# Performance work log

Hardware: AMD Instinct MI355X
Metric: run time of the kernel (lower is better)

## Reference

```python
import jax, jax.numpy as jnp
import numpy as np

D_MODEL = 1024
NHEAD = 16
WINDOW = 128


def setup_inputs() -> dict:
    key = jax.random.key(0)
    ks = jax.random.split(key, 7)
    B, L, D = 4, 4096, D_MODEL
    s = 0.02
    return {
        "q": jax.random.normal(ks[0], (B, L, D), jnp.float32),
        "k": jax.random.normal(ks[1], (B, L, D), jnp.float32),
        "v": jax.random.normal(ks[2], (B, L, D), jnp.float32),
        "in_proj_w": jax.random.normal(ks[3], (3 * D, D), jnp.float32) * s,
        "in_proj_b": jnp.zeros((3 * D,), jnp.float32),
        "out_w": jax.random.normal(ks[4], (D, D), jnp.float32) * s,
        "out_b": jnp.zeros((D,), jnp.float32),
    }


def reference(q, k, v, in_proj_w, in_proj_b, out_w, out_b):
    B, L, D = q.shape
    H, W = NHEAD, WINDOW
    hd = D // H
    nW = L // W
    Wq, Wk, Wv = in_proj_w[:D], in_proj_w[D:2 * D], in_proj_w[2 * D:]
    bq, bk, bv = in_proj_b[:D], in_proj_b[D:2 * D], in_proj_b[2 * D:]
    # shared per-window projections (same weights every window, as in nn.MultiheadAttention)
    qp = (q @ Wq.T + bq).reshape(B, nW, W, H, hd)
    kp = (k @ Wk.T + bk).reshape(B, nW, W, H, hd)
    vp = (v @ Wv.T + bv).reshape(B, nW, W, H, hd)
    scale = 1.0 / np.sqrt(hd).astype(np.float32)
    # block-diagonal attention: scores only within each window n
    scores = jnp.einsum("bnqhd,bnkhd->bnhqk", qp, kp) * scale  # [B,nW,H,W,W]
    attn = jax.nn.softmax(scores, axis=-1)
    out = jnp.einsum("bnhqk,bnkhd->bnqhd", attn, vp).reshape(B, L, D)
    return out @ out_w.T + out_b
```

## Files before the change

kernel.cpp:

```cpp
#include <hip/hip_runtime.h>


#define M_TOK 16384
#define DM    1024

typedef __bf16 bf16x8 __attribute__((ext_vector_type(8)));
typedef float  f32x4  __attribute__((ext_vector_type(4)));
typedef unsigned short us8 __attribute__((ext_vector_type(8)));
typedef unsigned short us4 __attribute__((ext_vector_type(4)));

__device__ __forceinline__ unsigned short f2bf(float f) {
    unsigned u = __float_as_uint(f);
    u += 0x7FFFu + ((u >> 16) & 1u);
    return (unsigned short)(u >> 16);
}

__global__ __launch_bounds__(256) void gemm_qkv(
    const float* __restrict__ qin, const float* __restrict__ kin,
    const float* __restrict__ vin, const float* __restrict__ ipw,
    const float* __restrict__ ipb, unsigned short* __restrict__ qkv)
{
    __shared__ unsigned short As[128 * 40];
    __shared__ unsigned short Ws[128 * 40];

    const int z = blockIdx.z;
    const float* A  = (z == 0) ? qin : ((z == 1) ? kin : vin);
    const float* Wp = ipw + (size_t)z * DM * DM;
    const float* bp = ipb + z * DM;
    unsigned short* Cp = qkv + (size_t)z * M_TOK * DM;

    const int mbase = blockIdx.y * 128;
    const int nbase = blockIdx.x * 128;
    const int tid  = threadIdx.x;
    const int lane = tid & 63;
    const int wv   = tid >> 6;
    const int wrow = (wv >> 1) * 64;
    const int wcol = (wv & 1) * 64;
    const int lrow = lane & 15;
    const int kof  = (lane >> 4) * 8;
    const int srow = tid >> 3;
    const int sc4  = tid & 7;

    f32x4 acc[4][4] = {};

    for (int ks = 0; ks < 32; ++ks) {
        const int k0 = ks * 32;
        __syncthreads();
        #pragma unroll
        for (int it = 0; it < 4; ++it) {
            int row = it * 32 + srow;
            float4 av = *(const float4*)(A  + (size_t)(mbase + row) * DM + k0 + sc4 * 4);
            float4 wf = *(const float4*)(Wp + (size_t)(nbase + row) * DM + k0 + sc4 * 4);
            us4 ap, wp4;
            ap[0] = f2bf(av.x); ap[1] = f2bf(av.y); ap[2] = f2bf(av.z); ap[3] = f2bf(av.w);
            wp4[0] = f2bf(wf.x); wp4[1] = f2bf(wf.y); wp4[2] = f2bf(wf.z); wp4[3] = f2bf(wf.w);
            *(us4*)(As + row * 40 + sc4 * 4) = ap;
            *(us4*)(Ws + row * 40 + sc4 * 4) = wp4;
        }
        __syncthreads();

        bf16x8 af[4], bfr[4];
        #pragma unroll
        for (int i = 0; i < 4; ++i)
            af[i] = *(const bf16x8*)(As + (wrow + i * 16 + lrow) * 40 + kof);
        #pragma unroll
        for (int i = 0; i < 4; ++i)
            bfr[i] = *(const bf16x8*)(Ws + (wcol + i * 16 + lrow) * 40 + kof);
        #pragma unroll
        for (int i = 0; i < 4; ++i)
            #pragma unroll
            for (int j = 0; j < 4; ++j)
                acc[i][j] = __builtin_amdgcn_mfma_f32_16x16x32_bf16(af[i], bfr[j], acc[i][j], 0, 0, 0);
    }

    #pragma unroll
    for (int j = 0; j < 4; ++j) {
        int gc = nbase + wcol + j * 16 + lrow;
        float bv = bp[gc];
        #pragma unroll
        for (int i = 0; i < 4; ++i) {
            int gr0 = mbase + wrow + i * 16 + (lane >> 4) * 4;
            #pragma unroll
            for (int r = 0; r < 4; ++r)
                Cp[(size_t)(gr0 + r) * DM + gc] = f2bf(acc[i][j][r] + bv);
        }
    }
}

__global__ __launch_bounds__(256) void gemm_out(
    const unsigned short* __restrict__ x, const float* __restrict__ ow,
    const float* __restrict__ ob, float* __restrict__ out)
{
    __shared__ unsigned short As[128 * 40];
    __shared__ unsigned short Ws[128 * 40];

    const int mbase = blockIdx.y * 128;
    const int nbase = blockIdx.x * 128;
    const int tid  = threadIdx.x;
    const int lane = tid & 63;
    const int wv   = tid >> 6;
    const int wrow = (wv >> 1) * 64;
    const int wcol = (wv & 1) * 64;
    const int lrow = lane & 15;
    const int kof  = (lane >> 4) * 8;
    const int srow = tid >> 3;
    const int sc4  = tid & 7;

    f32x4 acc[4][4] = {};

    for (int ks = 0; ks < 32; ++ks) {
        const int k0 = ks * 32;
        __syncthreads();
        #pragma unroll
        for (int it = 0; it < 4; ++it) {
            int row = it * 32 + srow;
            us4 av = *(const us4*)(x + (size_t)(mbase + row) * DM + k0 + sc4 * 4);
            float4 wf = *(const float4*)(ow + (size_t)(nbase + row) * DM + k0 + sc4 * 4);
            us4 wp4;
            wp4[0] = f2bf(wf.x); wp4[1] = f2bf(wf.y); wp4[2] = f2bf(wf.z); wp4[3] = f2bf(wf.w);
            *(us4*)(As + row * 40 + sc4 * 4) = av;
            *(us4*)(Ws + row * 40 + sc4 * 4) = wp4;
        }
        __syncthreads();

        bf16x8 af[4], bfr[4];
        #pragma unroll
        for (int i = 0; i < 4; ++i)
            af[i] = *(const bf16x8*)(As + (wrow + i * 16 + lrow) * 40 + kof);
        #pragma unroll
        for (int i = 0; i < 4; ++i)
            bfr[i] = *(const bf16x8*)(Ws + (wcol + i * 16 + lrow) * 40 + kof);
        #pragma unroll
        for (int i = 0; i < 4; ++i)
            #pragma unroll
            for (int j = 0; j < 4; ++j)
                acc[i][j] = __builtin_amdgcn_mfma_f32_16x16x32_bf16(af[i], bfr[j], acc[i][j], 0, 0, 0);
    }

    #pragma unroll
    for (int j = 0; j < 4; ++j) {
        int gc = nbase + wcol + j * 16 + lrow;
        float bv = ob[gc];
        #pragma unroll
        for (int i = 0; i < 4; ++i) {
            int gr0 = mbase + wrow + i * 16 + (lane >> 4) * 4;
            #pragma unroll
            for (int r = 0; r < 4; ++r)
                out[(size_t)(gr0 + r) * DM + gc] = acc[i][j][r] + bv;
        }
    }
}

__global__ __launch_bounds__(256) void attn_win(
    const unsigned short* __restrict__ qkv, unsigned short* __restrict__ aout)
{
    const unsigned short* qp = qkv;
    const unsigned short* kp = qkv + (size_t)M_TOK * DM;
    const unsigned short* vp = qkv + 2 * (size_t)M_TOK * DM;

    const int gid = blockIdx.x;
    const int h  = gid & 15;
    const int wi = (gid >> 4) & 31;
    const int b  = gid >> 9;
    const size_t rowbase = (size_t)b * 4096 + (size_t)wi * 128;

    const int tid  = threadIdx.x;
    const int lane = tid & 63;
    const int wv   = tid >> 6;
    const int lrow = lane & 15;
    const int kof  = (lane >> 4) * 8;

    __shared__ unsigned short sm[27136];
    unsigned short* Qs = sm;
    unsigned short* Ks = sm + 9216;
    unsigned short* Vt = sm + 18432;
    unsigned short* Ps = sm;

    {
        const int seg = tid & 7;
        #pragma unroll
        for (int it = 0; it < 4; ++it) {
            int r = it * 32 + (tid >> 3);
            size_t g = (rowbase + r) * DM + h * 64 + seg * 8;
            *(int4*)(Qs + r * 72 + seg * 8) = *(const int4*)(qp + g);
            *(int4*)(Ks + r * 72 + seg * 8) = *(const int4*)(kp + g);
        }
        #pragma unroll
        for (int it = 0; it < 4; ++it) {
            int j  = tid & 127;
            int sg = it * 2 + (tid >> 7);
            us8 vv = *(const us8*)(vp + (rowbase + j) * DM + h * 64 + sg * 8);
            #pragma unroll
            for (int d = 0; d < 8; ++d)
                Vt[(sg * 8 + d) * 136 + j] = vv[d];
        }
    }
    __syncthreads();

    f32x4 acc[2][8] = {};
    #pragma unroll
    for (int ki = 0; ki < 2; ++ki) {
        bf16x8 a0 = *(const bf16x8*)(Qs + (wv * 32 +  0 + lrow) * 72 + ki * 32 + kof);
        bf16x8 a1 = *(const bf16x8*)(Qs + (wv * 32 + 16 + lrow) * 72 + ki * 32 + kof);
        #pragma unroll
        for (int ni = 0; ni < 8; ++ni) {
            bf16x8 bb = *(const bf16x8*)(Ks + (ni * 16 + lrow) * 72 + ki * 32 + kof);
            acc[0][ni] = __builtin_amdgcn_mfma_f32_16x16x32_bf16(a0, bb, acc[0][ni], 0, 0, 0);
            acc[1][ni] = __builtin_amdgcn_mfma_f32_16x16x32_bf16(a1, bb, acc[1][ni], 0, 0, 0);
        }
    }

    const float scale = 0.125f;
    #pragma unroll
    for (int mi = 0; mi < 2; ++mi) {
        #pragma unroll
        for (int r = 0; r < 4; ++r) {
            float sc[8];
            float mx = -3.4e38f;
            #pragma unroll
            for (int ni = 0; ni < 8; ++ni) { sc[ni] = acc[mi][ni][r] * scale; mx = fmaxf(mx, sc[ni]); }
            mx = fmaxf(mx, __shfl_xor(mx, 1));
            mx = fmaxf(mx, __shfl_xor(mx, 2));
            mx = fmaxf(mx, __shfl_xor(mx, 4));
            mx = fmaxf(mx, __shfl_xor(mx, 8));
            float sum = 0.f;
            #pragma unroll
            for (int ni = 0; ni < 8; ++ni) { sc[ni] = __expf(sc[ni] - mx); sum += sc[ni]; }
            sum += __shfl_xor(sum, 1);
            sum += __shfl_xor(sum, 2);
            sum += __shfl_xor(sum, 4);
            sum += __shfl_xor(sum, 8);
            float inv = 1.0f / sum;
            #pragma unroll
            for (int ni = 0; ni < 8; ++ni) acc[mi][ni][r] = sc[ni] * inv;
        }
    }

    __syncthreads();

    #pragma unroll
    for (int mi = 0; mi < 2; ++mi)
        #pragma unroll
        for (int ni = 0; ni < 8; ++ni)
            #pragma unroll
            for (int r = 0; r < 4; ++r)
                Ps[(wv * 32 + mi * 16 + (lane >> 4) * 4 + r) * 136 + ni * 16 + lrow] =
                    f2bf(acc[mi][ni][r]);
    __syncthreads();

    f32x4 o[2][4] = {};
    #pragma unroll
    for (int kj = 0; kj < 4; ++kj) {
        bf16x8 a0 = *(const bf16x8*)(Ps + (wv * 32 +  0 + lrow) * 136 + kj * 32 + kof);
        bf16x8 a1 = *(const bf16x8*)(Ps + (wv * 32 + 16 + lrow) * 136 + kj * 32 + kof);
        #pragma unroll
        for (int nd = 0; nd < 4; ++nd) {
            bf16x8 bb = *(const bf16x8*)(Vt + (nd * 16 + lrow) * 136 + kj * 32 + kof);
            o[0][nd] = __builtin_amdgcn_mfma_f32_16x16x32_bf16(a0, bb, o[0][nd], 0, 0, 0);
            o[1][nd] = __builtin_amdgcn_mfma_f32_16x16x32_bf16(a1, bb, o[1][nd], 0, 0, 0);
        }
    }

    #pragma unroll
    for (int mi = 0; mi < 2; ++mi) {
        #pragma unroll
        for (int nd = 0; nd < 4; ++nd) {
            #pragma unroll
            for (int r = 0; r < 4; ++r) {
                int R = wv * 32 + mi * 16 + (lane >> 4) * 4 + r;
                int c = h * 64 + nd * 16 + lrow;
                aout[(rowbase + R) * DM + c] = f2bf(o[mi][nd][r]);
            }
        }
    }
}

extern "C" void kernel_launch(void* const* d_in, const int* in_sizes, int n_in,
                              void* d_out, int out_size, void* d_ws, size_t ws_size,
                              hipStream_t stream) {
    const float* q   = (const float*)d_in[0];
    const float* k   = (const float*)d_in[1];
    const float* v   = (const float*)d_in[2];
    const float* ipw = (const float*)d_in[3];
    const float* ipb = (const float*)d_in[4];
    const float* ow  = (const float*)d_in[5];
    const float* ob  = (const float*)d_in[6];
    float* out = (float*)d_out;

    unsigned short* qkv = (unsigned short*)d_ws;
    const size_t qkv_elems = 3ull * M_TOK * DM;
    const size_t need_full = (qkv_elems + (size_t)M_TOK * DM) * 2;
    unsigned short* aout = (ws_size >= need_full) ? qkv + qkv_elems : qkv;

    gemm_qkv<<<dim3(8, 128, 3), 256, 0, stream>>>(q, k, v, ipw, ipb, qkv);
    attn_win<<<dim3(2048), 256, 0, stream>>>(qkv, aout);
    gemm_out<<<dim3(8, 128), 256, 0, stream>>>(aout, ow, ob, out);
}
```

Baseline: 542.1 us.

## Pre-convert inputs to bf16, use direct global-to-LDS GEMM loads and head-major QKV layout

```diff
diff --git a/kernel.cpp b/kernel.cpp
--- a/kernel.cpp
+++ b/kernel.cpp
@@ -1,5 +1,4 @@
 #include <hip/hip_runtime.h>
-
 
 #define M_TOK 16384
 #define DM    1024
@@ -15,34 +14,241 @@
     return (unsigned short)(u >> 16);
 }
 
-__global__ __launch_bounds__(256) void gemm_qkv(
+__device__ __forceinline__ void gl2lds16(const unsigned short* g, unsigned short* l) {
+    __builtin_amdgcn_global_load_lds(
+        (const __attribute__((address_space(1))) unsigned int*)g,
+        (__attribute__((address_space(3))) unsigned int*)l, 16, 0, 0);
+}
+
+__global__ __launch_bounds__(256) void conv_f2b(
+    const float* __restrict__ src, unsigned short* __restrict__ dst, int n8)
+{
+    int i = blockIdx.x * blockDim.x + threadIdx.x;
+    int stride = gridDim.x * blockDim.x;
+    for (; i < n8; i += stride) {
+        const float4* s = (const float4*)(src + (size_t)i * 8);
+        float4 a = s[0], b = s[1];
+        us8 o;
+        o[0] = f2bf(a.x); o[1] = f2bf(a.y); o[2] = f2bf(a.z); o[3] = f2bf(a.w);
+        o[4] = f2bf(b.x); o[5] = f2bf(b.y); o[6] = f2bf(b.z); o[7] = f2bf(b.w);
+        *(us8*)(dst + (size_t)i * 8) = o;
+    }
+}
+
+#define GEMM_CORE(A_, B_)                                                      \
+    __shared__ unsigned short As[4096];                                        \
+    __shared__ unsigned short Bs[4096];                                        \
+    const int tid = threadIdx.x, lane = tid & 63, wv = tid >> 6;               \
+    const int wrow = (wv >> 1) * 64, wcol = (wv & 1) * 64;                     \
+    const int lrow = lane & 15, qd = lane >> 4;                                \
+    const int mbase = blockIdx.y * 128, nbase = blockIdx.x * 128;              \
+    const int s0 = tid, s1 = tid + 256;                                        \
+    const int r0 = s0 >> 2, c0 = (s0 & 3) ^ ((r0 >> 1) & 3);                   \
+    const int r1 = s1 >> 2, c1 = (s1 & 3) ^ ((r1 >> 1) & 3);                   \
+    const int g0 = r0 * DM + c0 * 8;                                           \
+    const int g1 = r1 * DM + c1 * 8;                                           \
+    int aslot[4], bslot[4];                                                    \
+    _Pragma("unroll")                                                          \
+    for (int i = 0; i < 4; ++i) {                                              \
+        int ra = wrow + i * 16 + lrow;                                         \
+        int rb = wcol + i * 16 + lrow;                                         \
+        aslot[i] = ra * 32 + (qd ^ ((ra >> 1) & 3)) * 8;                       \
+        bslot[i] = rb * 32 + (qd ^ ((rb >> 1) & 3)) * 8;                       \
+    }                                                                          \
+    const unsigned short* Ab = (A_) + (size_t)mbase * DM;                      \
+    const unsigned short* Bb = (B_) + (size_t)nbase * DM;                      \
+    f32x4 acc[4][4] = {};                                                      \
+    for (int k0 = 0; k0 < DM; k0 += 32) {                                      \
+        __syncthreads();                                                       \
+        gl2lds16(Ab + k0 + g0, As + s0 * 8);                                   \
+        gl2lds16(Ab + k0 + g1, As + s1 * 8);                                   \
+        gl2lds16(Bb + k0 + g0, Bs + s0 * 8);                                   \
+        gl2lds16(Bb + k0 + g1, Bs + s1 * 8);                                   \
+        __syncthreads();                                                       \
+        bf16x8 af[4], bfr[4];                                                  \
+        _Pragma("unroll")                                                      \
+        for (int i = 0; i < 4; ++i) af[i]  = *(const bf16x8*)(As + aslot[i]);  \
+        _Pragma("unroll")                                                      \
+        for (int i = 0; i < 4; ++i) bfr[i] = *(const bf16x8*)(Bs + bslot[i]);  \
+        _Pragma("unroll")                                                      \
+        for (int i = 0; i < 4; ++i)                                            \
+            _Pragma("unroll")                                                  \
+            for (int j = 0; j < 4; ++j)                                        \
+                acc[i][j] = __builtin_amdgcn_mfma_f32_16x16x32_bf16(           \
+                    af[i], bfr[j], acc[i][j], 0, 0, 0);                        \
+    }
+
+__global__ __launch_bounds__(256) void gemm_bt_qkv(
+    const unsigned short* __restrict__ A, const unsigned short* __restrict__ W,
+    const float* __restrict__ bias, unsigned short* __restrict__ C, int z)
+{
+    GEMM_CORE(A, W)
+    if (z <= 1) {
+        #pragma unroll
+        for (int j = 0; j < 4; ++j) {
+            int gc = nbase + wcol + j * 16 + lrow;
+            int h = gc >> 6, dh = gc & 63;
+            float bv = bias[gc];
+            #pragma unroll
+            for (int i = 0; i < 4; ++i) {
+                int gr0 = mbase + wrow + i * 16 + qd * 4;
+                int b = gr0 >> 12;
+                #pragma unroll
+                for (int r = 0; r < 4; ++r) {
+                    int tok = (gr0 + r) & 4095;
+                    C[(((size_t)b * 16 + h) * 4096 + tok) * 64 + dh] =
+                        f2bf(acc[i][j][r] + bv);
+                }
+            }
+        }
+    } else {
+        #pragma unroll
+        for (int j = 0; j < 4; ++j) {
+            int gc = nbase + wcol + j * 16 + lrow;
+            int h = gc >> 6, dh = gc & 63;
+            float bv = bias[gc];
+            #pragma unroll
+            for (int i = 0; i < 4; ++i) {
+                int gr0 = mbase + wrow + i * 16 + qd * 4;
+                int b = gr0 >> 12, tok = gr0 & 4095;
+                us4 pk;
+                #pragma unroll
+                for (int r = 0; r < 4; ++r) pk[r] = f2bf(acc[i][j][r] + bv);
+                *(us4*)(C + (((size_t)b * 16 + h) * 64 + dh) * 4096 + tok) = pk;
+            }
+        }
+    }
+}
+
+__global__ __launch_bounds__(256) void gemm_bt_out(
+    const unsigned short* __restrict__ A, const unsigned short* __restrict__ W,
+    const float* __restrict__ bias, float* __restrict__ out)
+{
+    GEMM_CORE(A, W)
+    #pragma unroll
+    for (int j = 0; j < 4; ++j) {
+        int gc = nbase + wcol + j * 16 + lrow;
+        float bv = bias[gc];
+        #pragma unroll
+        for (int i = 0; i < 4; ++i) {
+            int gr0 = mbase + wrow + i * 16 + qd * 4;
+            #pragma unroll
+            for (int r = 0; r < 4; ++r)
+                out[(size_t)(gr0 + r) * DM + gc] = acc[i][j][r] + bv;
+        }
+    }
+}
+
+__global__ __launch_bounds__(256) void attn_v2(
+    const unsigned short* __restrict__ qh, const unsigned short* __restrict__ kh,
+    const unsigned short* __restrict__ vt, unsigned short* __restrict__ aout)
+{
+    const int gid = blockIdx.x;
+    const int h  = gid & 15;
+    const int wi = (gid >> 4) & 31;
+    const int b  = gid >> 9;
+    const int bh = b * 16 + h;
+
+    const unsigned short* Qp = qh + ((size_t)bh * 4096 + wi * 128) * 64;
+    const unsigned short* Kp = kh + ((size_t)bh * 4096 + wi * 128) * 64;
+    const unsigned short* Vp = vt + (size_t)bh * 64 * 4096 + wi * 128;
+
+    const int tid = threadIdx.x, lane = tid & 63, wv = tid >> 6;
+    const int lrow = lane & 15, qd = lane >> 4, kof = qd * 8;
+
+    __shared__ unsigned short Ps[128 * 136];
+
+    f32x4 acc[2][8] = {};
+    #pragma unroll
+    for (int ki = 0; ki < 2; ++ki) {
+        bf16x8 a0 = *(const bf16x8*)(Qp + (wv * 32 +  0 + lrow) * 64 + ki * 32 + kof);
+        bf16x8 a1 = *(const bf16x8*)(Qp + (wv * 32 + 16 + lrow) * 64 + ki * 32 + kof);
+        #pragma unroll
+        for (int ni = 0; ni < 8; ++ni) {
+            bf16x8 bb = *(const bf16x8*)(Kp + (ni * 16 + lrow) * 64 + ki * 32 + kof);
+            acc[0][ni] = __builtin_amdgcn_mfma_f32_16x16x32_bf16(a0, bb, acc[0][ni], 0, 0, 0);
+            acc[1][ni] = __builtin_amdgcn_mfma_f32_16x16x32_bf16(a1, bb, acc[1][ni], 0, 0, 0);
+        }
+    }
+
+    const float scale = 0.125f;
+    #pragma unroll
+    for (int mi = 0; mi < 2; ++mi) {
+        #pragma unroll
+        for (int r = 0; r < 4; ++r) {
+            float sc[8];
+            float mx = -3.4e38f;
+            #pragma unroll
+            for (int ni = 0; ni < 8; ++ni) { sc[ni] = acc[mi][ni][r] * scale; mx = fmaxf(mx, sc[ni]); }
+            mx = fmaxf(mx, __shfl_xor(mx, 1));
+            mx = fmaxf(mx, __shfl_xor(mx, 2));
+            mx = fmaxf(mx, __shfl_xor(mx, 4));
+            mx = fmaxf(mx, __shfl_xor(mx, 8));
+            float sum = 0.f;
+            #pragma unroll
+            for (int ni = 0; ni < 8; ++ni) { sc[ni] = __expf(sc[ni] - mx); sum += sc[ni]; }
+            sum += __shfl_xor(sum, 1);
+            sum += __shfl_xor(sum, 2);
+            sum += __shfl_xor(sum, 4);
+            sum += __shfl_xor(sum, 8);
+            float inv = 1.0f / sum;
+            #pragma unroll
+            for (int ni = 0; ni < 8; ++ni) acc[mi][ni][r] = sc[ni] * inv;
+        }
+    }
+
+    #pragma unroll
+    for (int mi = 0; mi < 2; ++mi)
+        #pragma unroll
+        for (int ni = 0; ni < 8; ++ni)
+            #pragma unroll
+            for (int r = 0; r < 4; ++r)
+                Ps[(wv * 32 + mi * 16 + qd * 4 + r) * 136 + ni * 16 + lrow] =
+                    f2bf(acc[mi][ni][r]);
+
+    f32x4 o[2][4] = {};
+    #pragma unroll
+    for (int kj = 0; kj < 4; ++kj) {
+        bf16x8 a0 = *(const bf16x8*)(Ps + (wv * 32 +  0 + lrow) * 136 + kj * 32 + kof);
+        bf16x8 a1 = *(const bf16x8*)(Ps + (wv * 32 + 16 + lrow) * 136 + kj * 32 + kof);
+        #pragma unroll
+        for (int nd = 0; nd < 4; ++nd) {
+            bf16x8 bb = *(const bf16x8*)(Vp + (size_t)(nd * 16 + lrow) * 4096 + kj * 32 + kof);
+            o[0][nd] = __builtin_amdgcn_mfma_f32_16x16x32_bf16(a0, bb, o[0][nd], 0, 0, 0);
+            o[1][nd] = __builtin_amdgcn_mfma_f32_16x16x32_bf16(a1, bb, o[1][nd], 0, 0, 0);
+        }
+    }
+
+    #pragma unroll
+    for (int mi = 0; mi < 2; ++mi)
+        #pragma unroll
+        for (int nd = 0; nd < 4; ++nd)
+            #pragma unroll
+            for (int r = 0; r < 4; ++r) {
+                int R = wv * 32 + mi * 16 + qd * 4 + r;
+                int c = h * 64 + nd * 16 + lrow;
+                aout[(size_t)(b * 4096 + wi * 128 + R) * DM + c] = f2bf(o[mi][nd][r]);
+            }
+}
+
+__global__ __launch_bounds__(256) void gemm_qkv_v1(
     const float* __restrict__ qin, const float* __restrict__ kin,
     const float* __restrict__ vin, const float* __restrict__ ipw,
     const float* __restrict__ ipb, unsigned short* __restrict__ qkv)
 {
     __shared__ unsigned short As[128 * 40];
     __shared__ unsigned short Ws[128 * 40];
-
     const int z = blockIdx.z;
     const float* A  = (z == 0) ? qin : ((z == 1) ? kin : vin);
     const float* Wp = ipw + (size_t)z * DM * DM;
     const float* bp = ipb + z * DM;
     unsigned short* Cp = qkv + (size_t)z * M_TOK * DM;
-
-    const int mbase = blockIdx.y * 128;
-    const int nbase = blockIdx.x * 128;
-    const int tid  = threadIdx.x;
-    const int lane = tid & 63;
-    const int wv   = tid >> 6;
-    const int wrow = (wv >> 1) * 64;
-    const int wcol = (wv & 1) * 64;
-    const int lrow = lane & 15;
-    const int kof  = (lane >> 4) * 8;
-    const int srow = tid >> 3;
-    const int sc4  = tid & 7;
-
+    const int mbase = blockIdx.y * 128, nbase = blockIdx.x * 128;
+    const int tid = threadIdx.x, lane = tid & 63, wv = tid >> 6;
+    const int wrow = (wv >> 1) * 64, wcol = (wv & 1) * 64;
+    const int lrow = lane & 15, kof = (lane >> 4) * 8;
+    const int srow = tid >> 3, sc4 = tid & 7;
     f32x4 acc[4][4] = {};
-
     for (int ks = 0; ks < 32; ++ks) {
         const int k0 = ks * 32;
         __syncthreads();
@@ -58,21 +264,17 @@
             *(us4*)(Ws + row * 40 + sc4 * 4) = wp4;
         }
         __syncthreads();
-
         bf16x8 af[4], bfr[4];
         #pragma unroll
-        for (int i = 0; i < 4; ++i)
-            af[i] = *(const bf16x8*)(As + (wrow + i * 16 + lrow) * 40 + kof);
-        #pragma unroll
-        for (int i = 0; i < 4; ++i)
-            bfr[i] = *(const bf16x8*)(Ws + (wcol + i * 16 + lrow) * 40 + kof);
+        for (int i = 0; i < 4; ++i) af[i]  = *(const bf16x8*)(As + (wrow + i * 16 + lrow) * 40 + kof);
+        #pragma unroll
+        for (int i = 0; i < 4; ++i) bfr[i] = *(const bf16x8*)(Ws + (wcol + i * 16 + lrow) * 40 + kof);
         #pragma unroll
         for (int i = 0; i < 4; ++i)
             #pragma unroll
             for (int j = 0; j < 4; ++j)
                 acc[i][j] = __builtin_amdgcn_mfma_f32_16x16x32_bf16(af[i], bfr[j], acc[i][j], 0, 0, 0);
     }
-
     #pragma unroll
     for (int j = 0; j < 4; ++j) {
         int gc = nbase + wcol + j * 16 + lrow;
@@ -87,27 +289,18 @@
     }
 }
 
-__global__ __launch_bounds__(256) void gemm_out(
+__global__ __launch_bounds__(256) void gemm_out_v1(
     const unsigned short* __restrict__ x, const float* __restrict__ ow,
     const float* __restrict__ ob, float* __restrict__ out)
 {
     __shared__ unsigned short As[128 * 40];
     __shared__ unsigned short Ws[128 * 40];
-
-    const int mbase = blockIdx.y * 128;
-    const int nbase = blockIdx.x * 128;
-    const int tid  = threadIdx.x;
-    const int lane = tid & 63;
-    const int wv   = tid >> 6;
-    const int wrow = (wv >> 1) * 64;
-    const int wcol = (wv & 1) * 64;
-    const int lrow = lane & 15;
-    const int kof  = (lane >> 4) * 8;
-    const int srow = tid >> 3;
-    const int sc4  = tid & 7;
-
+    const int mbase = blockIdx.y * 128, nbase = blockIdx.x * 128;
+    const int tid = threadIdx.x, lane = tid & 63, wv = tid >> 6;
+    const int wrow = (wv >> 1) * 64, wcol = (wv & 1) * 64;
+    const int lrow = lane & 15, kof = (lane >> 4) * 8;
+    const int srow = tid >> 3, sc4 = tid & 7;
     f32x4 acc[4][4] = {};
-
     for (int ks = 0; ks < 32; ++ks) {
         const int k0 = ks * 32;
         __syncthreads();
@@ -122,21 +315,17 @@
             *(us4*)(Ws + row * 40 + sc4 * 4) = wp4;
         }
         __syncthreads();
-
         bf16x8 af[4], bfr[4];
         #pragma unroll
-        for (int i = 0; i < 4; ++i)
-            af[i] = *(const bf16x8*)(As + (wrow + i * 16 + lrow) * 40 + kof);
-        #pragma unroll
-        for (int i = 0; i < 4; ++i)
-            bfr[i] = *(const bf16x8*)(Ws + (wcol + i * 16 + lrow) * 40 + kof);
+        for (int i = 0; i < 4; ++i) af[i]  = *(const bf16x8*)(As + (wrow + i * 16 + lrow) * 40 + kof);
+        #pragma unroll
+        for (int i = 0; i < 4; ++i) bfr[i] = *(const bf16x8*)(Ws + (wcol + i * 16 + lrow) * 40 + kof);
         #pragma unroll
         for (int i = 0; i < 4; ++i)
             #pragma unroll
             for (int j = 0; j < 4; ++j)
                 acc[i][j] = __builtin_amdgcn_mfma_f32_16x16x32_bf16(af[i], bfr[j], acc[i][j], 0, 0, 0);
     }
-
     #pragma unroll
     for (int j = 0; j < 4; ++j) {
         int gc = nbase + wcol + j * 16 + lrow;
@@ -151,31 +340,22 @@
     }
 }
 
-__global__ __launch_bounds__(256) void attn_win(
+__global__ __launch_bounds__(256) void attn_win_v1(
     const unsigned short* __restrict__ qkv, unsigned short* __restrict__ aout)
 {
     const unsigned short* qp = qkv;
     const unsigned short* kp = qkv + (size_t)M_TOK * DM;
     const unsigned short* vp = qkv + 2 * (size_t)M_TOK * DM;
-
     const int gid = blockIdx.x;
-    const int h  = gid & 15;
-    const int wi = (gid >> 4) & 31;
-    const int b  = gid >> 9;
+    const int h = gid & 15, wi = (gid >> 4) & 31, b = gid >> 9;
     const size_t rowbase = (size_t)b * 4096 + (size_t)wi * 128;
-
-    const int tid  = threadIdx.x;
-    const int lane = tid & 63;
-    const int wv   = tid >> 6;
-    const int lrow = lane & 15;
-    const int kof  = (lane >> 4) * 8;
-
+    const int tid = threadIdx.x, lane = tid & 63, wv = tid >> 6;
+    const int lrow = lane & 15, kof = (lane >> 4) * 8;
     __shared__ unsigned short sm[27136];
     unsigned short* Qs = sm;
     unsigned short* Ks = sm + 9216;
     unsigned short* Vt = sm + 18432;
     unsigned short* Ps = sm;
-
     {
         const int seg = tid & 7;
         #pragma unroll
@@ -187,16 +367,14 @@
         }
         #pragma unroll
         for (int it = 0; it < 4; ++it) {
-            int j  = tid & 127;
+            int j = tid & 127;
             int sg = it * 2 + (tid >> 7);
             us8 vv = *(const us8*)(vp + (rowbase + j) * DM + h * 64 + sg * 8);
             #pragma unroll
-            for (int d = 0; d < 8; ++d)
-                Vt[(sg * 8 + d) * 136 + j] = vv[d];
+            for (int d = 0; d < 8; ++d) Vt[(sg * 8 + d) * 136 + j] = vv[d];
         }
     }
     __syncthreads();
-
     f32x4 acc[2][8] = {};
     #pragma unroll
     for (int ki = 0; ki < 2; ++ki) {
@@ -209,7 +387,6 @@
             acc[1][ni] = __builtin_amdgcn_mfma_f32_16x16x32_bf16(a1, bb, acc[1][ni], 0, 0, 0);
         }
     }
-
     const float scale = 0.125f;
     #pragma unroll
     for (int mi = 0; mi < 2; ++mi) {
@@ -219,25 +396,19 @@
             float mx = -3.4e38f;
             #pragma unroll
             for (int ni = 0; ni < 8; ++ni) { sc[ni] = acc[mi][ni][r] * scale; mx = fmaxf(mx, sc[ni]); }
-            mx = fmaxf(mx, __shfl_xor(mx, 1));
-            mx = fmaxf(mx, __shfl_xor(mx, 2));
-            mx = fmaxf(mx, __shfl_xor(mx, 4));
-            mx = fmaxf(mx, __shfl_xor(mx, 8));
+            mx = fmaxf(mx, __shfl_xor(mx, 1)); mx = fmaxf(mx, __shfl_xor(mx, 2));
+            mx = fmaxf(mx, __shfl_xor(mx, 4)); mx = fmaxf(mx, __shfl_xor(mx, 8));
             float sum = 0.f;
             #pragma unroll
             for (int ni = 0; ni < 8; ++ni) { sc[ni] = __expf(sc[ni] - mx); sum += sc[ni]; }
-            sum += __shfl_xor(sum, 1);
-            sum += __shfl_xor(sum, 2);
-            sum += __shfl_xor(sum, 4);
-            sum += __shfl_xor(sum, 8);
+            sum += __shfl_xor(sum, 1); sum += __shfl_xor(sum, 2);
+            sum += __shfl_xor(sum, 4); sum += __shfl_xor(sum, 8);
             float inv = 1.0f / sum;
             #pragma unroll
             for (int ni = 0; ni < 8; ++ni) acc[mi][ni][r] = sc[ni] * inv;
         }
     }
-
     __syncthreads();
-
     #pragma unroll
     for (int mi = 0; mi < 2; ++mi)
         #pragma unroll
@@ -247,7 +418,6 @@
                 Ps[(wv * 32 + mi * 16 + (lane >> 4) * 4 + r) * 136 + ni * 16 + lrow] =
                     f2bf(acc[mi][ni][r]);
     __syncthreads();
-
     f32x4 o[2][4] = {};
     #pragma unroll
     for (int kj = 0; kj < 4; ++kj) {
@@ -260,19 +430,16 @@
             o[1][nd] = __builtin_amdgcn_mfma_f32_16x16x32_bf16(a1, bb, o[1][nd], 0, 0, 0);
         }
     }
-
-    #pragma unroll
-    for (int mi = 0; mi < 2; ++mi) {
-        #pragma unroll
-        for (int nd = 0; nd < 4; ++nd) {
+    #pragma unroll
+    for (int mi = 0; mi < 2; ++mi)
+        #pragma unroll
+        for (int nd = 0; nd < 4; ++nd)
             #pragma unroll
             for (int r = 0; r < 4; ++r) {
                 int R = wv * 32 + mi * 16 + (lane >> 4) * 4 + r;
                 int c = h * 64 + nd * 16 + lrow;
                 aout[(rowbase + R) * DM + c] = f2bf(o[mi][nd][r]);
             }
-        }
-    }
 }
 
 extern "C" void kernel_launch(void* const* d_in, const int* in_sizes, int n_in,
@@ -287,12 +454,36 @@
     const float* ob  = (const float*)d_in[6];
     float* out = (float*)d_out;
 
-    unsigned short* qkv = (unsigned short*)d_ws;
-    const size_t qkv_elems = 3ull * M_TOK * DM;
-    const size_t need_full = (qkv_elems + (size_t)M_TOK * DM) * 2;
-    unsigned short* aout = (ws_size >= need_full) ? qkv + qkv_elems : qkv;
-
-    gemm_qkv<<<dim3(8, 128, 3), 256, 0, stream>>>(q, k, v, ipw, ipb, qkv);
-    attn_win<<<dim3(2048), 256, 0, stream>>>(qkv, aout);
-    gemm_out<<<dim3(8, 128), 256, 0, stream>>>(aout, ow, ob, out);
-}
+    const size_t MD = (size_t)M_TOK * DM;
+    const size_t WW = (size_t)DM * DM;
+    const size_t need = (4 * MD + 3 * WW) * 2;
+
+    if (ws_size >= need) {
+        unsigned short* X   = (unsigned short*)d_ws;
+        unsigned short* qh  = X + MD;
+        unsigned short* kh  = X + 2 * MD;
+        unsigned short* vtb = X + 3 * MD;
+        unsigned short* Wb  = X + 4 * MD;
+        unsigned short* aout = X;
+        unsigned short* OwB  = Wb;
+
+        conv_f2b<<<1536, 256, 0, stream>>>(ipw, Wb, (int)(3 * WW / 8));
+        conv_f2b<<<8192, 256, 0, stream>>>(q, X, (int)(MD / 8));
+        gemm_bt_qkv<<<dim3(8, 128), 256, 0, stream>>>(X, Wb, ipb, qh, 0);
+        conv_f2b<<<8192, 256, 0, stream>>>(k, X, (int)(MD / 8));
+        gemm_bt_qkv<<<dim3(8, 128), 256, 0, stream>>>(X, Wb + WW, ipb + DM, kh, 1);
+        conv_f2b<<<8192, 256, 0, stream>>>(v, X, (int)(MD / 8));
+        gemm_bt_qkv<<<dim3(8, 128), 256, 0, stream>>>(X, Wb + 2 * WW, ipb + 2 * DM, vtb, 2);
+        conv_f2b<<<512, 256, 0, stream>>>(ow, OwB, (int)(WW / 8));
+        attn_v2<<<2048, 256, 0, stream>>>(qh, kh, vtb, aout);
+        gemm_bt_out<<<dim3(8, 128), 256, 0, stream>>>(aout, OwB, ob, out);
+    } else {
+        unsigned short* qkv = (unsigned short*)d_ws;
+        const size_t qkv_elems = 3 * MD;
+        const size_t need_full = (qkv_elems + MD) * 2;
+        unsigned short* aout = (ws_size >= need_full) ? qkv + qkv_elems : qkv;
+        gemm_qkv_v1<<<dim3(8, 128, 3), 256, 0, stream>>>(q, k, v, ipw, ipb, qkv);
+        attn_win_v1<<<2048, 256, 0, stream>>>(qkv, aout);
+        gemm_out_v1<<<dim3(8, 128), 256, 0, stream>>>(aout, ow, ob, out);
+    }
+}
```

New measurement: 493.6 us. -8.9%, faster.

## Pre-convert weights to bf16, head-major QKV layout, direct-global attention, XCD swizzle

Applied to the files above, without the earlier changes.

```diff
diff --git a/kernel.cpp b/kernel.cpp
--- a/kernel.cpp
+++ b/kernel.cpp
@@ -1,5 +1,4 @@
 #include <hip/hip_runtime.h>
-
 
 #define M_TOK 16384
 #define DM    1024
@@ -15,126 +14,175 @@
     return (unsigned short)(u >> 16);
 }
 
-__global__ __launch_bounds__(256) void gemm_qkv(
+__device__ __forceinline__ unsigned pk2bf(float a, float b) {
+#if __has_builtin(__builtin_amdgcn_cvt_pk_bf16_f32)
+    auto r = __builtin_amdgcn_cvt_pk_bf16_f32(a, b);
+    unsigned u; __builtin_memcpy(&u, &r, 4); return u;
+#else
+    return (unsigned)f2bf(a) | ((unsigned)f2bf(b) << 16);
+#endif
+}
+
+__device__ __forceinline__ void gl2lds16(const unsigned short* g, unsigned short* l) {
+    __builtin_amdgcn_global_load_lds(
+        (const __attribute__((address_space(1))) unsigned int*)g,
+        (__attribute__((address_space(3))) unsigned int*)l, 16, 0, 0);
+}
+
+__device__ __forceinline__ void stage_f32slot(
+    const float* __restrict__ gsrc, unsigned short* lds, int s, int k0)
+{
+    int r = s >> 2, c = (s & 3) ^ ((r >> 1) & 3);
+    const float4* p = (const float4*)(gsrc + (size_t)r * DM + k0 + c * 8);
+    float4 f0 = p[0], f1 = p[1];
+    uint4 o;
+    o.x = pk2bf(f0.x, f0.y);
+    o.y = pk2bf(f0.z, f0.w);
+    o.z = pk2bf(f1.x, f1.y);
+    o.w = pk2bf(f1.z, f1.w);
+    *(uint4*)(lds + s * 8) = o;
+}
+
+__global__ __launch_bounds__(256) void conv_f2b(
+    const float* __restrict__ src, unsigned short* __restrict__ dst, int n8)
+{
+    int i = blockIdx.x * blockDim.x + threadIdx.x;
+    int stride = gridDim.x * blockDim.x;
+    for (; i < n8; i += stride) {
+        const float4* s = (const float4*)(src + (size_t)i * 8);
+        float4 a = s[0], b = s[1];
+        uint4 o;
+        o.x = pk2bf(a.x, a.y); o.y = pk2bf(a.z, a.w);
+        o.z = pk2bf(b.x, b.y); o.w = pk2bf(b.z, b.w);
+        *(uint4*)(dst + (size_t)i * 8) = o;
+    }
+}
+
+#define XCD_SWIZZLE()                                                          \
+    const int fid = blockIdx.x + (blockIdx.y << 3);                            \
+    const int mbase = (((fid & 7) << 4) + (fid >> 6)) << 7;                    \
+    const int nbase = ((fid >> 3) & 7) << 7;
+
+#define GEMM_IDX()                                                             \
+    const int tid = threadIdx.x, lane = tid & 63, wv = tid >> 6;               \
+    const int wrow = (wv >> 1) * 64, wcol = (wv & 1) * 64;                     \
+    const int lrow = lane & 15, qd = lane >> 4;                                \
+    const int s0 = tid, s1 = tid + 256;                                        \
+    const int r0 = s0 >> 2, c0 = (s0 & 3) ^ ((r0 >> 1) & 3);                   \
+    const int r1 = s1 >> 2, c1 = (s1 & 3) ^ ((r1 >> 1) & 3);                   \
+    const int g0 = r0 * DM + c0 * 8;                                           \
+    const int g1 = r1 * DM + c1 * 8;                                           \
+    int aslot[4], bslot[4];                                                    \
+    _Pragma("unroll")                                                          \
+    for (int i = 0; i < 4; ++i) {                                              \
+        int ra = wrow + i * 16 + lrow;                                         \
+        int rb = wcol + i * 16 + lrow;                                         \
+        aslot[i] = ra * 32 + (qd ^ ((ra >> 1) & 3)) * 8;                       \
+        bslot[i] = rb * 32 + (qd ^ ((rb >> 1) & 3)) * 8;                       \
+    }
+
+#define GEMM_MFMA_BLOCK()                                                      \
+    bf16x8 af[4], bfr[4];                                                      \
+    _Pragma("unroll")                                                          \
+    for (int i = 0; i < 4; ++i) af[i]  = *(const bf16x8*)(As + aslot[i]);      \
+    _Pragma("unroll")                                                          \
+    for (int i = 0; i < 4; ++i) bfr[i] = *(const bf16x8*)(Bs + bslot[i]);      \
+    _Pragma("unroll")                                                          \
+    for (int i = 0; i < 4; ++i)                                                \
+        _Pragma("unroll")                                                      \
+        for (int j = 0; j < 4; ++j)                                            \
+            acc[i][j] = __builtin_amdgcn_mfma_f32_16x16x32_bf16(               \
+                af[i], bfr[j], acc[i][j], 0, 0, 0);
+
+__global__ __launch_bounds__(256) void gemm_qkv_f32(
     const float* __restrict__ qin, const float* __restrict__ kin,
-    const float* __restrict__ vin, const float* __restrict__ ipw,
-    const float* __restrict__ ipb, unsigned short* __restrict__ qkv)
-{
-    __shared__ unsigned short As[128 * 40];
-    __shared__ unsigned short Ws[128 * 40];
+    const float* __restrict__ vin, const unsigned short* __restrict__ Wb,
+    const float* __restrict__ ipb, unsigned short* __restrict__ Cq,
+    unsigned short* __restrict__ Ck, unsigned short* __restrict__ Cv)
+{
+    __shared__ unsigned short As[4096];
+    __shared__ unsigned short Bs[4096];
+    XCD_SWIZZLE()
+    GEMM_IDX()
 
     const int z = blockIdx.z;
-    const float* A  = (z == 0) ? qin : ((z == 1) ? kin : vin);
-    const float* Wp = ipw + (size_t)z * DM * DM;
+    const float* A = (z == 0) ? qin : ((z == 1) ? kin : vin);
+    const unsigned short* W = Wb + (size_t)z * DM * DM;
     const float* bp = ipb + z * DM;
-    unsigned short* Cp = qkv + (size_t)z * M_TOK * DM;
-
-    const int mbase = blockIdx.y * 128;
-    const int nbase = blockIdx.x * 128;
-    const int tid  = threadIdx.x;
-    const int lane = tid & 63;
-    const int wv   = tid >> 6;
-    const int wrow = (wv >> 1) * 64;
-    const int wcol = (wv & 1) * 64;
-    const int lrow = lane & 15;
-    const int kof  = (lane >> 4) * 8;
-    const int srow = tid >> 3;
-    const int sc4  = tid & 7;
+
+    const float* Ab = A + (size_t)mbase * DM;
+    const unsigned short* Bb = W + (size_t)nbase * DM;
 
     f32x4 acc[4][4] = {};
-
-    for (int ks = 0; ks < 32; ++ks) {
-        const int k0 = ks * 32;
+    for (int k0 = 0; k0 < DM; k0 += 32) {
         __syncthreads();
-        #pragma unroll
-        for (int it = 0; it < 4; ++it) {
-            int row = it * 32 + srow;
-            float4 av = *(const float4*)(A  + (size_t)(mbase + row) * DM + k0 + sc4 * 4);
-            float4 wf = *(const float4*)(Wp + (size_t)(nbase + row) * DM + k0 + sc4 * 4);
-            us4 ap, wp4;
-            ap[0] = f2bf(av.x); ap[1] = f2bf(av.y); ap[2] = f2bf(av.z); ap[3] = f2bf(av.w);
-            wp4[0] = f2bf(wf.x); wp4[1] = f2bf(wf.y); wp4[2] = f2bf(wf.z); wp4[3] = f2bf(wf.w);
-            *(us4*)(As + row * 40 + sc4 * 4) = ap;
-            *(us4*)(Ws + row * 40 + sc4 * 4) = wp4;
-        }
+        gl2lds16(Bb + k0 + g0, Bs + s0 * 8);
+        gl2lds16(Bb + k0 + g1, Bs + s1 * 8);
+        stage_f32slot(Ab, As, s0, k0);
+        stage_f32slot(Ab, As, s1, k0);
         __syncthreads();
-
-        bf16x8 af[4], bfr[4];
-        #pragma unroll
-        for (int i = 0; i < 4; ++i)
-            af[i] = *(const bf16x8*)(As + (wrow + i * 16 + lrow) * 40 + kof);
-        #pragma unroll
-        for (int i = 0; i < 4; ++i)
-            bfr[i] = *(const bf16x8*)(Ws + (wcol + i * 16 + lrow) * 40 + kof);
-        #pragma unroll
-        for (int i = 0; i < 4; ++i)
-            #pragma unroll
-            for (int j = 0; j < 4; ++j)
-                acc[i][j] = __builtin_amdgcn_mfma_f32_16x16x32_bf16(af[i], bfr[j], acc[i][j], 0, 0, 0);
-    }
-
-    #pragma unroll
-    for (int j = 0; j < 4; ++j) {
-        int gc = nbase + wcol + j * 16 + lrow;
-        float bv = bp[gc];
-        #pragma unroll
-        for (int i = 0; i < 4; ++i) {
-            int gr0 = mbase + wrow + i * 16 + (lane >> 4) * 4;
-            #pragma unroll
-            for (int r = 0; r < 4; ++r)
-                Cp[(size_t)(gr0 + r) * DM + gc] = f2bf(acc[i][j][r] + bv);
-        }
-    }
-}
-
-__global__ __launch_bounds__(256) void gemm_out(
-    const unsigned short* __restrict__ x, const float* __restrict__ ow,
+        GEMM_MFMA_BLOCK()
+    }
+
+    if (z <= 1) {
+        unsigned short* C = (z == 0) ? Cq : Ck;
+        #pragma unroll
+        for (int j = 0; j < 4; ++j) {
+            int gc = nbase + wcol + j * 16 + lrow;
+            int h = gc >> 6, dh = gc & 63;
+            float bv = bp[gc];
+            #pragma unroll
+            for (int i = 0; i < 4; ++i) {
+                int gr0 = mbase + wrow + i * 16 + qd * 4;
+                int b = gr0 >> 12;
+                #pragma unroll
+                for (int r = 0; r < 4; ++r) {
+                    int tok = (gr0 + r) & 4095;
+                    C[(((size_t)b * 16 + h) * 4096 + tok) * 64 + dh] =
+                        f2bf(acc[i][j][r] + bv);
+                }
+            }
+        }
+    } else {
+        #pragma unroll
+        for (int j = 0; j < 4; ++j) {
+            int gc = nbase + wcol + j * 16 + lrow;
+            int h = gc >> 6, dh = gc & 63;
+            float bv = bp[gc];
+            #pragma unroll
+            for (int i = 0; i < 4; ++i) {
+                int gr0 = mbase + wrow + i * 16 + qd * 4;
+                int b = gr0 >> 12, tok = gr0 & 4095;
+                us4 pk;
+                #pragma unroll
+                for (int r = 0; r < 4; ++r) pk[r] = f2bf(acc[i][j][r] + bv);
+                *(us4*)(Cv + (((size_t)b * 16 + h) * 64 + dh) * 4096 + tok) = pk;
+            }
+        }
+    }
+}
+
+__global__ __launch_bounds__(256) void gemm_bt_out(
+    const unsigned short* __restrict__ Ab16, const float* __restrict__ ow,
     const float* __restrict__ ob, float* __restrict__ out)
 {
-    __shared__ unsigned short As[128 * 40];
-    __shared__ unsigned short Ws[128 * 40];
-
-    const int mbase = blockIdx.y * 128;
-    const int nbase = blockIdx.x * 128;
-    const int tid  = threadIdx.x;
-    const int lane = tid & 63;
-    const int wv   = tid >> 6;
-    const int wrow = (wv >> 1) * 64;
-    const int wcol = (wv & 1) * 64;
-    const int lrow = lane & 15;
-    const int kof  = (lane >> 4) * 8;
-    const int srow = tid >> 3;
-    const int sc4  = tid & 7;
+    __shared__ unsigned short As[4096];
+    __shared__ unsigned short Bs[4096];
+    XCD_SWIZZLE()
+    GEMM_IDX()
+
+    const unsigned short* Ab = Ab16 + (size_t)mbase * DM;
+    const float* Bb = ow + (size_t)nbase * DM;
 
     f32x4 acc[4][4] = {};
-
-    for (int ks = 0; ks < 32; ++ks) {
-        const int k0 = ks * 32;
+    for (int k0 = 0; k0 < DM; k0 += 32) {
         __syncthreads();
-        #pragma unroll
-        for (int it = 0; it < 4; ++it) {
-            int row = it * 32 + srow;
-            us4 av = *(const us4*)(x + (size_t)(mbase + row) * DM + k0 + sc4 * 4);
-            float4 wf = *(const float4*)(ow + (size_t)(nbase + row) * DM + k0 + sc4 * 4);
-            us4 wp4;
-            wp4[0] = f2bf(wf.x); wp4[1] = f2bf(wf.y); wp4[2] = f2bf(wf.z); wp4[3] = f2bf(wf.w);
-            *(us4*)(As + row * 40 + sc4 * 4) = av;
-            *(us4*)(Ws + row * 40 + sc4 * 4) = wp4;
-        }
+        gl2lds16(Ab + k0 + g0, As + s0 * 8);
+        gl2lds16(Ab + k0 + g1, As + s1 * 8);
+        stage_f32slot(Bb, Bs, s0, k0);
+        stage_f32slot(Bb, Bs, s1, k0);
         __syncthreads();
-
-        bf16x8 af[4], bfr[4];
-        #pragma unroll
-        for (int i = 0; i < 4; ++i)
-            af[i] = *(const bf16x8*)(As + (wrow + i * 16 + lrow) * 40 + kof);
-        #pragma unroll
-        for (int i = 0; i < 4; ++i)
-            bfr[i] = *(const bf16x8*)(Ws + (wcol + i * 16 + lrow) * 40 + kof);
-        #pragma unroll
-        for (int i = 0; i < 4; ++i)
-            #pragma unroll
-            for (int j = 0; j < 4; ++j)
-                acc[i][j] = __builtin_amdgcn_mfma_f32_16x16x32_bf16(af[i], bfr[j], acc[i][j], 0, 0, 0);
+        GEMM_MFMA_BLOCK()
     }
 
     #pragma unroll
@@ -143,7 +191,7 @@
         float bv = ob[gc];
         #pragma unroll
         for (int i = 0; i < 4; ++i) {
-            int gr0 = mbase + wrow + i * 16 + (lane >> 4) * 4;
+            int gr0 = mbase + wrow + i * 16 + qd * 4;
             #pragma unroll
             for (int r = 0; r < 4; ++r)
                 out[(size_t)(gr0 + r) * DM + gc] = acc[i][j][r] + bv;
@@ -151,60 +199,33 @@
     }
 }
 
-__global__ __launch_bounds__(256) void attn_win(
-    const unsigned short* __restrict__ qkv, unsigned short* __restrict__ aout)
-{
-    const unsigned short* qp = qkv;
-    const unsigned short* kp = qkv + (size_t)M_TOK * DM;
-    const unsigned short* vp = qkv + 2 * (size_t)M_TOK * DM;
-
+__global__ __launch_bounds__(256) void attn_v2(
+    const unsigned short* __restrict__ qh, const unsigned short* __restrict__ kh,
+    const unsigned short* __restrict__ vt, unsigned short* __restrict__ aout)
+{
     const int gid = blockIdx.x;
     const int h  = gid & 15;
     const int wi = (gid >> 4) & 31;
     const int b  = gid >> 9;
-    const size_t rowbase = (size_t)b * 4096 + (size_t)wi * 128;
-
-    const int tid  = threadIdx.x;
-    const int lane = tid & 63;
-    const int wv   = tid >> 6;
-    const int lrow = lane & 15;
-    const int kof  = (lane >> 4) * 8;
-
-    __shared__ unsigned short sm[27136];
-    unsigned short* Qs = sm;
-    unsigned short* Ks = sm + 9216;
-    unsigned short* Vt = sm + 18432;
-    unsigned short* Ps = sm;
-
-    {
-        const int seg = tid & 7;
-        #pragma unroll
-        for (int it = 0; it < 4; ++it) {
-            int r = it * 32 + (tid >> 3);
-            size_t g = (rowbase + r) * DM + h * 64 + seg * 8;
-            *(int4*)(Qs + r * 72 + seg * 8) = *(const int4*)(qp + g);
-            *(int4*)(Ks + r * 72 + seg * 8) = *(const int4*)(kp + g);
-        }
-        #pragma unroll
-        for (int it = 0; it < 4; ++it) {
-            int j  = tid & 127;
-            int sg = it * 2 + (tid >> 7);
-            us8 vv = *(const us8*)(vp + (rowbase + j) * DM + h * 64 + sg * 8);
-            #pragma unroll
-            for (int d = 0; d < 8; ++d)
-                Vt[(sg * 8 + d) * 136 + j] = vv[d];
-        }
-    }
-    __syncthreads();
+    const int bh = b * 16 + h;
+
+    const unsigned short* Qp = qh + ((size_t)bh * 4096 + wi * 128) * 64;
+    const unsigned short* Kp = kh + ((size_t)bh * 4096 + wi * 128) * 64;
+    const unsigned short* Vp = vt + (size_t)bh * 64 * 4096 + wi * 128;
+
+    const int tid = threadIdx.x, lane = tid & 63, wv = tid >> 6;
+    const int lrow = lane & 15, qd = lane >> 4, kof = qd * 8;
+
+    __shared__ unsigned short Ps[128 * 136];
 
     f32x4 acc[2][8] = {};
     #pragma unroll
     for (int ki = 0; ki < 2; ++ki) {
-        bf16x8 a0 = *(const bf16x8*)(Qs + (wv * 32 +  0 + lrow) * 72 + ki * 32 + kof);
-        bf16x8 a1 = *(const bf16x8*)(Qs + (wv * 32 + 16 + lrow) * 72 + ki * 32 + kof);
+        bf16x8 a0 = *(const bf16x8*)(Qp + (wv * 32 +  0 + lrow) * 64 + ki * 32 + kof);
+        bf16x8 a1 = *(const bf16x8*)(Qp + (wv * 32 + 16 + lrow) * 64 + ki * 32 + kof);
         #pragma unroll
         for (int ni = 0; ni < 8; ++ni) {
-            bf16x8 bb = *(const bf16x8*)(Ks + (ni * 16 + lrow) * 72 + ki * 32 + kof);
+            bf16x8 bb = *(const bf16x8*)(Kp + (ni * 16 + lrow) * 64 + ki * 32 + kof);
             acc[0][ni] = __builtin_amdgcn_mfma_f32_16x16x32_bf16(a0, bb, acc[0][ni], 0, 0, 0);
             acc[1][ni] = __builtin_amdgcn_mfma_f32_16x16x32_bf16(a1, bb, acc[1][ni], 0, 0, 0);
         }
@@ -236,17 +257,14 @@
         }
     }
 
-    __syncthreads();
-
     #pragma unroll
     for (int mi = 0; mi < 2; ++mi)
         #pragma unroll
         for (int ni = 0; ni < 8; ++ni)
             #pragma unroll
             for (int r = 0; r < 4; ++r)
-                Ps[(wv * 32 + mi * 16 + (lane >> 4) * 4 + r) * 136 + ni * 16 + lrow] =
+                Ps[(wv * 32 + mi * 16 + qd * 4 + r) * 136 + ni * 16 + lrow] =
                     f2bf(acc[mi][ni][r]);
-    __syncthreads();
 
     f32x4 o[2][4] = {};
     #pragma unroll
@@ -255,24 +273,22 @@
         bf16x8 a1 = *(const bf16x8*)(Ps + (wv * 32 + 16 + lrow) * 136 + kj * 32 + kof);
         #pragma unroll
         for (int nd = 0; nd < 4; ++nd) {
-            bf16x8 bb = *(const bf16x8*)(Vt + (nd * 16 + lrow) * 136 + kj * 32 + kof);
+            bf16x8 bb = *(const bf16x8*)(Vp + (size_t)(nd * 16 + lrow) * 4096 + kj * 32 + kof);
             o[0][nd] = __builtin_amdgcn_mfma_f32_16x16x32_bf16(a0, bb, o[0][nd], 0, 0, 0);
             o[1][nd] = __builtin_amdgcn_mfma_f32_16x16x32_bf16(a1, bb, o[1][nd], 0, 0, 0);
         }
     }
 
     #pragma unroll
-    for (int mi = 0; mi < 2; ++mi) {
-        #pragma unroll
-        for (int nd = 0; nd < 4; ++nd) {
+    for (int mi = 0; mi < 2; ++mi)
+        #pragma unroll
+        for (int nd = 0; nd < 4; ++nd)
             #pragma unroll
             for (int r = 0; r < 4; ++r) {
-                int R = wv * 32 + mi * 16 + (lane >> 4) * 4 + r;
+                int R = wv * 32 + mi * 16 + qd * 4 + r;
                 int c = h * 64 + nd * 16 + lrow;
-                aout[(rowbase + R) * DM + c] = f2bf(o[mi][nd][r]);
+                aout[(size_t)(b * 4096 + wi * 128 + R) * DM + c] = f2bf(o[mi][nd][r]);
             }
-        }
-    }
 }
 
 extern "C" void kernel_launch(void* const* d_in, const int* in_sizes, int n_in,
@@ -287,12 +303,17 @@
     const float* ob  = (const float*)d_in[6];
     float* out = (float*)d_out;
 
-    unsigned short* qkv = (unsigned short*)d_ws;
-    const size_t qkv_elems = 3ull * M_TOK * DM;
-    const size_t need_full = (qkv_elems + (size_t)M_TOK * DM) * 2;
-    unsigned short* aout = (ws_size >= need_full) ? qkv + qkv_elems : qkv;
-
-    gemm_qkv<<<dim3(8, 128, 3), 256, 0, stream>>>(q, k, v, ipw, ipb, qkv);
-    attn_win<<<dim3(2048), 256, 0, stream>>>(qkv, aout);
-    gemm_out<<<dim3(8, 128), 256, 0, stream>>>(aout, ow, ob, out);
-}
+    const size_t MD = (size_t)M_TOK * DM;
+    const size_t WW = (size_t)DM * DM;
+
+    unsigned short* qh   = (unsigned short*)d_ws;
+    unsigned short* kh   = qh + MD;
+    unsigned short* vtb  = qh + 2 * MD;
+    unsigned short* aout = qh + 3 * MD;
+    unsigned short* Wb   = qh + 4 * MD;
+
+    conv_f2b<<<1536, 256, 0, stream>>>(ipw, Wb, (int)(3 * WW / 8));
+    gemm_qkv_f32<<<dim3(8, 128, 3), 256, 0, stream>>>(q, k, v, Wb, ipb, qh, kh, vtb);
+    attn_v2<<<2048, 256, 0, stream>>>(qh, kh, vtb, aout);
+    gemm_bt_out<<<dim3(8, 128), 256, 0, stream>>>(aout, ow, ob, out);
+}
```

Result: slower. 577.0 us (+6.4%).
